# Kernel optimization log

Hardware: AMD Instinct MI355X
Metric: run time of the kernel (lower is better)

The kernel has to match this reference:

```python
import jax, jax.numpy as jnp
import numpy as np

B, N, D_IN, D_OUT, E = 2, 50000, 64, 64, 800000
EPS = 0.0


def setup_inputs() -> dict:
    key = jax.random.key(0)
    ks = jax.random.split(key, 6)
    x = jax.random.normal(ks[0], (B, N, D_IN), dtype=jnp.float32)
    edge_index = jax.random.randint(ks[1], (2, E), 0, N, dtype=jnp.int64)
    # Linear params stored as [in, out] so y = h @ W + b (same math as torch Linear)
    W1 = jax.random.normal(ks[2], (D_IN, D_OUT), dtype=jnp.float32) * (1.0 / np.sqrt(D_IN))
    b1 = jax.random.normal(ks[3], (D_OUT,), dtype=jnp.float32) * 0.01
    W2 = jax.random.normal(ks[4], (D_OUT, D_OUT), dtype=jnp.float32) * (1.0 / np.sqrt(D_OUT))
    b2 = jax.random.normal(ks[5], (D_OUT,), dtype=jnp.float32) * 0.01
    return {"x": x, "edge_index": edge_index, "W1": W1, "b1": b1, "W2": W2, "b2": b2}


def reference(x, edge_index, W1, b1, W2, b2):
    src, dst = edge_index[0], edge_index[1]
    # GIN aggregation: agg[b, d] += x[b, s] for every edge (s, d), vectorized
    # gather messages [B, E, D] then scatter-add into [B, N, D]
    agg = jnp.zeros_like(x).at[:, dst].add(x[:, src])
    h = (1.0 + EPS) * x + agg
    h = jax.nn.relu(h @ W1 + b1)
    out = h @ W2 + b2
    return out
```

## Files before the change

kernel.cpp:

```cpp
#include <hip/hip_runtime.h>


#define N_NODES 50000
#define N_EDGES 800000
#define DIM 64
#define NROWS (2 * N_NODES)
#define CAP 64
#define CSTRIDE 16

#define WS_PAD_NEEDED  22400000u
#define WS_BF16_NEEDED 19400704u
#define WS_CAP_NEEDED  13000704u

typedef __attribute__((ext_vector_type(8))) short bf16x8;
typedef __attribute__((ext_vector_type(4))) float f32x4;

__device__ __forceinline__ float rlanef(float v, int l) {
    return __int_as_float(__builtin_amdgcn_readlane(__float_as_int(v), l));
}
__device__ __forceinline__ short f2bf(float f) {
    unsigned u = __float_as_uint(f);
    return (short)((u + 0x7FFFu + ((u >> 16) & 1u)) >> 16);
}
__device__ __forceinline__ unsigned pack2bf(float lo, float hi) {
    return (unsigned)(unsigned short)f2bf(lo) | ((unsigned)(unsigned short)f2bf(hi) << 16);
}

__global__ __launch_bounds__(256)
void k_fill_cap_cvt(const int* __restrict__ ei, const float* __restrict__ x,
                    unsigned* __restrict__ counts,
                    unsigned short* __restrict__ adj,
                    unsigned* __restrict__ xbp) {
    const int tid = blockIdx.x * 256 + threadIdx.x;

    const float4 f0 = reinterpret_cast<const float4*>(x)[tid * 2];
    const float4 f1 = reinterpret_cast<const float4*>(x)[tid * 2 + 1];
    uint4 p;
    p.x = pack2bf(f0.x, f0.y);
    p.y = pack2bf(f0.z, f0.w);
    p.z = pack2bf(f1.x, f1.y);
    p.w = pack2bf(f1.z, f1.w);
    reinterpret_cast<uint4*>(xbp)[tid] = p;

    if (tid < N_EDGES) {
        int s = ei[tid];
        int d = ei[N_EDGES + tid];
        unsigned pos = atomicAdd(&counts[(size_t)d * CSTRIDE], 1u);
        if (pos < CAP) adj[(size_t)d * CAP + pos] = (unsigned short)s;
    }
}

__global__ __launch_bounds__(256, 8)
void k_gather_cap_bf16(const float* __restrict__ x,
                       const unsigned* __restrict__ xbp,
                       const unsigned* __restrict__ counts,
                       const unsigned short* __restrict__ adj,
                       float* __restrict__ out) {
    const int t = threadIdx.x;
    const int lane = t & 63;
    const int wave = t >> 6;
    const int node0 = (blockIdx.x * 4 + wave) * 4;

    const int half = lane >> 5;
    const int dpq  = lane & 31;
    const size_t bro = (size_t)half * N_NODES;

#define ULO(u) __uint_as_float((u) << 16)
#define UHI(u) __uint_as_float((u) & 0xFFFF0000u)

    #pragma unroll
    for (int j = 0; j < 4; ++j) {
        const int d = node0 + j;
        unsigned c = counts[(size_t)d * CSTRIDE];
        if (c > (unsigned)CAP) c = CAP;
        unsigned iv = 0u;
        if ((unsigned)lane < c)
            iv = (unsigned)adj[(size_t)d * CAP + lane];

        const float2 sv = *reinterpret_cast<const float2*>(
            x + (bro + (size_t)d) * DIM + dpq * 2);
        float ax = sv.x, ay = sv.y;

        for (unsigned k = 0; k < c; k += 8u) {
            const unsigned i0 = (unsigned)__builtin_amdgcn_readlane((int)iv, k);
            const unsigned i1 = (unsigned)__builtin_amdgcn_readlane((int)iv, k + 1);
            const unsigned i2 = (unsigned)__builtin_amdgcn_readlane((int)iv, k + 2);
            const unsigned i3 = (unsigned)__builtin_amdgcn_readlane((int)iv, k + 3);
            const unsigned i4 = (unsigned)__builtin_amdgcn_readlane((int)iv, k + 4);
            const unsigned i5 = (unsigned)__builtin_amdgcn_readlane((int)iv, k + 5);
            const unsigned i6 = (unsigned)__builtin_amdgcn_readlane((int)iv, k + 6);
            const unsigned i7 = (unsigned)__builtin_amdgcn_readlane((int)iv, k + 7);
            unsigned u0 = xbp[(bro + (size_t)i0) * 32 + dpq];
            unsigned u1 = xbp[(bro + (size_t)i1) * 32 + dpq];
            unsigned u2 = xbp[(bro + (size_t)i2) * 32 + dpq];
            unsigned u3 = xbp[(bro + (size_t)i3) * 32 + dpq];
            unsigned u4 = xbp[(bro + (size_t)i4) * 32 + dpq];
            unsigned u5 = xbp[(bro + (size_t)i5) * 32 + dpq];
            unsigned u6 = xbp[(bro + (size_t)i6) * 32 + dpq];
            unsigned u7 = xbp[(bro + (size_t)i7) * 32 + dpq];
            if (k + 1u >= c) u1 = 0u;
            if (k + 2u >= c) u2 = 0u;
            if (k + 3u >= c) u3 = 0u;
            if (k + 4u >= c) u4 = 0u;
            if (k + 5u >= c) u5 = 0u;
            if (k + 6u >= c) u6 = 0u;
            if (k + 7u >= c) u7 = 0u;
            ax += ((ULO(u0) + ULO(u1)) + (ULO(u2) + ULO(u3)))
                + ((ULO(u4) + ULO(u5)) + (ULO(u6) + ULO(u7)));
            ay += ((UHI(u0) + UHI(u1)) + (UHI(u2) + UHI(u3)))
                + ((UHI(u4) + UHI(u5)) + (UHI(u6) + UHI(u7)));
        }

        float2 r; r.x = ax; r.y = ay;
        *reinterpret_cast<float2*>(out + (bro + (size_t)d) * DIM + dpq * 2) = r;
    }
#undef ULO
#undef UHI
}

#define LPAD 72

__global__ __launch_bounds__(512)
void k_mlp_mfma(float* __restrict__ buf,
                const float* __restrict__ W1, const float* __restrict__ b1,
                const float* __restrict__ W2, const float* __restrict__ b2) {
    __shared__ short w1T[DIM * LPAD];
    __shared__ short w2T[DIM * LPAD];
    __shared__ float b1s[DIM], b2s[DIM];
    __shared__ short hT[8 * 16 * LPAD];

    const int t = threadIdx.x;
    for (int i = t; i < DIM * DIM; i += 512) {
        const int k = i >> 6, n = i & 63;
        w1T[n * LPAD + k] = f2bf(W1[i]);
        w2T[n * LPAD + k] = f2bf(W2[i]);
    }
    if (t < DIM) { b1s[t] = b1[t]; b2s[t] = b2[t]; }
    __syncthreads();

    const int lane = t & 63;
    const int wave = t >> 6;
    const int base = (blockIdx.x * 8 + wave) * 16;
    if (base >= NROWS) return;

    short* __restrict__ hw = hT + wave * 16 * LPAD;
    const int arow = lane & 15;
    const int kb   = (lane >> 4) * 8;
    const int crow = (lane >> 4) * 4;

    const float* hp = buf + (size_t)(base + arow) * DIM + kb;
    float4 u0 = *(const float4*)(hp);
    float4 u1 = *(const float4*)(hp + 4);
    float4 u2 = *(const float4*)(hp + 32);
    float4 u3 = *(const float4*)(hp + 36);
    bf16x8 a0, a1;
    a0[0] = f2bf(u0.x); a0[1] = f2bf(u0.y); a0[2] = f2bf(u0.z); a0[3] = f2bf(u0.w);
    a0[4] = f2bf(u1.x); a0[5] = f2bf(u1.y); a0[6] = f2bf(u1.z); a0[7] = f2bf(u1.w);
    a1[0] = f2bf(u2.x); a1[1] = f2bf(u2.y); a1[2] = f2bf(u2.z); a1[3] = f2bf(u2.w);
    a1[4] = f2bf(u3.x); a1[5] = f2bf(u3.y); a1[6] = f2bf(u3.z); a1[7] = f2bf(u3.w);

    #pragma unroll
    for (int nt = 0; nt < 4; ++nt) {
        const int col = nt * 16 + arow;
        const bf16x8 b0 = *(const bf16x8*)(w1T + col * LPAD + kb);
        const bf16x8 b1f = *(const bf16x8*)(w1T + col * LPAD + kb + 32);
        f32x4 acc = {0.f, 0.f, 0.f, 0.f};
        acc = __builtin_amdgcn_mfma_f32_16x16x32_bf16(a0, b0, acc, 0, 0, 0);
        acc = __builtin_amdgcn_mfma_f32_16x16x32_bf16(a1, b1f, acc, 0, 0, 0);
        const float bv = b1s[col];
        #pragma unroll
        for (int r = 0; r < 4; ++r) {
            float hv = fmaxf(acc[r] + bv, 0.0f);
            hw[(crow + r) * LPAD + col] = f2bf(hv);
        }
    }

    asm volatile("s_waitcnt lgkmcnt(0)" ::: "memory");
    __builtin_amdgcn_sched_barrier(0);

    const bf16x8 c0 = *(const bf16x8*)(hw + arow * LPAD + kb);
    const bf16x8 c1 = *(const bf16x8*)(hw + arow * LPAD + kb + 32);
    #pragma unroll
    for (int nt = 0; nt < 4; ++nt) {
        const int col = nt * 16 + arow;
        const bf16x8 b0 = *(const bf16x8*)(w2T + col * LPAD + kb);
        const bf16x8 b1f = *(const bf16x8*)(w2T + col * LPAD + kb + 32);
        f32x4 acc = {0.f, 0.f, 0.f, 0.f};
        acc = __builtin_amdgcn_mfma_f32_16x16x32_bf16(c0, b0, acc, 0, 0, 0);
        acc = __builtin_amdgcn_mfma_f32_16x16x32_bf16(c1, b1f, acc, 0, 0, 0);
        const float bv = b2s[col];
        #pragma unroll
        for (int r = 0; r < 4; ++r)
            buf[(size_t)(base + crow + r) * DIM + col] = acc[r] + bv;
    }
}

__global__ __launch_bounds__(256)
void k_fill_cap_cvt_r13(const int* __restrict__ ei, const float* __restrict__ x,
                        unsigned* __restrict__ counts,
                        unsigned short* __restrict__ adj,
                        unsigned* __restrict__ xbp) {
    const int tid = blockIdx.x * 256 + threadIdx.x;
    const float4 f0 = reinterpret_cast<const float4*>(x)[tid * 2];
    const float4 f1 = reinterpret_cast<const float4*>(x)[tid * 2 + 1];
    uint4 p;
    p.x = pack2bf(f0.x, f0.y);
    p.y = pack2bf(f0.z, f0.w);
    p.z = pack2bf(f1.x, f1.y);
    p.w = pack2bf(f1.z, f1.w);
    reinterpret_cast<uint4*>(xbp)[tid] = p;
    if (tid < N_EDGES) {
        int s = ei[tid];
        int d = ei[N_EDGES + tid];
        unsigned pos = atomicAdd(&counts[d], 1u);
        if (pos < CAP) adj[(size_t)d * CAP + pos] = (unsigned short)s;
    }
}

__global__ __launch_bounds__(256, 8)
void k_gather_cap_bf16_r13(const float* __restrict__ x,
                           const unsigned* __restrict__ xbp,
                           const unsigned* __restrict__ counts,
                           const unsigned short* __restrict__ adj,
                           float* __restrict__ out) {
    const int t = threadIdx.x;
    const int lane = t & 63;
    const int wave = t >> 6;
    const int node0 = (blockIdx.x * 4 + wave) * 4;
    const int half = lane >> 5;
    const int dpq  = lane & 31;
    const size_t bro = (size_t)half * N_NODES;
#define ULO(u) __uint_as_float((u) << 16)
#define UHI(u) __uint_as_float((u) & 0xFFFF0000u)
    #pragma unroll
    for (int j = 0; j < 4; ++j) {
        const int d = node0 + j;
        unsigned c = counts[d];
        if (c > (unsigned)CAP) c = CAP;
        unsigned iv = 0u;
        if ((unsigned)lane < c) iv = (unsigned)adj[(size_t)d * CAP + lane];
        const float2 sv = *reinterpret_cast<const float2*>(
            x + (bro + (size_t)d) * DIM + dpq * 2);
        float ax = sv.x, ay = sv.y;
        for (unsigned k = 0; k < c; k += 8u) {
            const unsigned i0 = (unsigned)__builtin_amdgcn_readlane((int)iv, k);
            const unsigned i1 = (unsigned)__builtin_amdgcn_readlane((int)iv, k + 1);
            const unsigned i2 = (unsigned)__builtin_amdgcn_readlane((int)iv, k + 2);
            const unsigned i3 = (unsigned)__builtin_amdgcn_readlane((int)iv, k + 3);
            const unsigned i4 = (unsigned)__builtin_amdgcn_readlane((int)iv, k + 4);
            const unsigned i5 = (unsigned)__builtin_amdgcn_readlane((int)iv, k + 5);
            const unsigned i6 = (unsigned)__builtin_amdgcn_readlane((int)iv, k + 6);
            const unsigned i7 = (unsigned)__builtin_amdgcn_readlane((int)iv, k + 7);
            unsigned u0 = xbp[(bro + (size_t)i0) * 32 + dpq];
            unsigned u1 = xbp[(bro + (size_t)i1) * 32 + dpq];
            unsigned u2 = xbp[(bro + (size_t)i2) * 32 + dpq];
            unsigned u3 = xbp[(bro + (size_t)i3) * 32 + dpq];
            unsigned u4 = xbp[(bro + (size_t)i4) * 32 + dpq];
            unsigned u5 = xbp[(bro + (size_t)i5) * 32 + dpq];
            unsigned u6 = xbp[(bro + (size_t)i6) * 32 + dpq];
            unsigned u7 = xbp[(bro + (size_t)i7) * 32 + dpq];
            if (k + 1u >= c) u1 = 0u;
            if (k + 2u >= c) u2 = 0u;
            if (k + 3u >= c) u3 = 0u;
            if (k + 4u >= c) u4 = 0u;
            if (k + 5u >= c) u5 = 0u;
            if (k + 6u >= c) u6 = 0u;
            if (k + 7u >= c) u7 = 0u;
            ax += ((ULO(u0) + ULO(u1)) + (ULO(u2) + ULO(u3)))
                + ((ULO(u4) + ULO(u5)) + (ULO(u6) + ULO(u7)));
            ay += ((UHI(u0) + UHI(u1)) + (UHI(u2) + UHI(u3)))
                + ((UHI(u4) + UHI(u5)) + (UHI(u6) + UHI(u7)));
        }
        float2 r; r.x = ax; r.y = ay;
        *reinterpret_cast<float2*>(out + (bro + (size_t)d) * DIM + dpq * 2) = r;
    }
#undef ULO
#undef UHI
}

__global__ __launch_bounds__(256)
void gin_scatter(const float* __restrict__ x, const int* __restrict__ ei,
                 float* __restrict__ agg) {
    unsigned tid = blockIdx.x * 256u + threadIdx.x;
    unsigned e = tid >> 5;
    if (e >= N_EDGES) return;
    unsigned d = (tid & 31u) * 2u;
    int s = ei[e];
    int dst = ei[N_EDGES + e];
    const float2 v0 = *reinterpret_cast<const float2*>(x + (size_t)s * DIM + d);
    float* a0 = agg + (size_t)dst * DIM + d;
    unsafeAtomicAdd(a0, v0.x);
    unsafeAtomicAdd(a0 + 1, v0.y);
    const float2 v1 = *reinterpret_cast<const float2*>(x + (size_t)(N_NODES + s) * DIM + d);
    float* a1 = agg + (size_t)(N_NODES + dst) * DIM + d;
    unsafeAtomicAdd(a1, v1.x);
    unsafeAtomicAdd(a1 + 1, v1.y);
}

__global__ __launch_bounds__(256)
void gin_mlp(float* __restrict__ buf,
             const float* __restrict__ W1, const float* __restrict__ b1,
             const float* __restrict__ W2, const float* __restrict__ b2) {
    __shared__ float w1s[DIM * DIM];
    __shared__ float w2s[DIM * DIM];
    __shared__ float b1sF[DIM], b2sF[DIM];
    const int t = threadIdx.x;
    for (int i = t; i < 1024; i += 256) {
        reinterpret_cast<float4*>(w1s)[i] = reinterpret_cast<const float4*>(W1)[i];
        reinterpret_cast<float4*>(w2s)[i] = reinterpret_cast<const float4*>(W2)[i];
    }
    if (t < DIM) { b1sF[t] = b1[t]; b2sF[t] = b2[t]; }
    __syncthreads();
    const int lane = t & 63;
    const int wave = t >> 6;
    const size_t row0 = ((size_t)blockIdx.x * 4 + wave) * 8;
    float xr[8], h[8], o[8];
    #pragma unroll
    for (int j = 0; j < 8; ++j) xr[j] = buf[(row0 + j) * DIM + lane];
    #pragma unroll
    for (int j = 0; j < 8; ++j) h[j] = b1sF[lane];
    #pragma unroll
    for (int k = 0; k < DIM; ++k) {
        float w = w1s[k * DIM + lane];
        #pragma unroll
        for (int j = 0; j < 8; ++j) h[j] = fmaf(rlanef(xr[j], k), w, h[j]);
    }
    #pragma unroll
    for (int j = 0; j < 8; ++j) h[j] = fmaxf(h[j], 0.0f);
    #pragma unroll
    for (int j = 0; j < 8; ++j) o[j] = b2sF[lane];
    #pragma unroll
    for (int k = 0; k < DIM; ++k) {
        float w = w2s[k * DIM + lane];
        #pragma unroll
        for (int j = 0; j < 8; ++j) o[j] = fmaf(rlanef(h[j], k), w, o[j]);
    }
    #pragma unroll
    for (int j = 0; j < 8; ++j) buf[(row0 + j) * DIM + lane] = o[j];
}

extern "C" void kernel_launch(void* const* d_in, const int* in_sizes, int n_in,
                              void* d_out, int out_size, void* d_ws, size_t ws_size,
                              hipStream_t stream) {
    const float* x  = (const float*)d_in[0];
    const int*   ei = (const int*)d_in[1];
    const float* W1 = (const float*)d_in[2];
    const float* b1 = (const float*)d_in[3];
    const float* W2 = (const float*)d_in[4];
    const float* b2 = (const float*)d_in[5];
    float* out = (float*)d_out;

    if (ws_size >= WS_PAD_NEEDED) {
        unsigned*       counts = (unsigned*)d_ws;
        unsigned short* adj16  = (unsigned short*)((char*)d_ws + 3200000);
        unsigned*       xbp    = (unsigned*)((char*)d_ws + 9600000);
        hipMemsetAsync(counts, 0, 3200000, stream);
        k_fill_cap_cvt<<<3125, 256, 0, stream>>>(ei, x, counts, adj16, xbp);
        k_gather_cap_bf16<<<N_NODES / 16, 256, 0, stream>>>(x, xbp, counts, adj16, out);
        k_mlp_mfma<<<(NROWS + 127) / 128, 512, 0, stream>>>(out, W1, b1, W2, b2);
    } else if (ws_size >= WS_BF16_NEEDED) {
        unsigned*       counts = (unsigned*)d_ws;
        unsigned short* adj16  = (unsigned short*)((char*)d_ws + 200704);
        unsigned*       xbp    = (unsigned*)((char*)d_ws + 6600704);
        hipMemsetAsync(counts, 0, N_NODES * sizeof(unsigned), stream);
        k_fill_cap_cvt_r13<<<3125, 256, 0, stream>>>(ei, x, counts, adj16, xbp);
        k_gather_cap_bf16_r13<<<N_NODES / 16, 256, 0, stream>>>(x, xbp, counts, adj16, out);
        k_mlp_mfma<<<(NROWS + 127) / 128, 512, 0, stream>>>(out, W1, b1, W2, b2);
    } else {
        hipMemcpyAsync(out, x, sizeof(float) * (size_t)NROWS * DIM,
                       hipMemcpyDeviceToDevice, stream);
        gin_scatter<<<(N_EDGES * 32 + 255) / 256, 256, 0, stream>>>(x, ei, out);
        gin_mlp<<<NROWS / 32, 256, 0, stream>>>(out, W1, b1, W2, b2);
    }
}
```

Before: 103.5 us.

## Fuse neighbor gather with MFMA MLP, keeping aggregated rows in LDS

The separate gather and MLP kernels are merged into one kernel. Each 512-thread block aggregates 64 nodes for both batches and writes the sums as packed bf16 into shared memory, then runs the two bf16 MFMA layers directly from LDS and writes only the final output. This removes the fp32 round trip of the aggregated tensor through global memory and one kernel launch. In exchange, every block repeats the weight transpose and conversion, LDS use per block grows, and the gather loop is no longer unrolled. The fallback branch for medium workspace sizes is also removed.

```diff
diff --git a/kernel.cpp b/kernel.cpp
--- a/kernel.cpp
+++ b/kernel.cpp
@@ -9,15 +9,10 @@
 #define CSTRIDE 16
 
 #define WS_PAD_NEEDED  22400000u
-#define WS_BF16_NEEDED 19400704u
-#define WS_CAP_NEEDED  13000704u
 
 typedef __attribute__((ext_vector_type(8))) short bf16x8;
 typedef __attribute__((ext_vector_type(4))) float f32x4;
 
-__device__ __forceinline__ float rlanef(float v, int l) {
-    return __int_as_float(__builtin_amdgcn_readlane(__float_as_int(v), l));
-}
 __device__ __forceinline__ short f2bf(float f) {
     unsigned u = __float_as_uint(f);
     return (short)((u + 0x7FFFu + ((u >> 16) & 1u)) >> 16);
@@ -50,27 +45,46 @@
     }
 }
 
-__global__ __launch_bounds__(256, 8)
-void k_gather_cap_bf16(const float* __restrict__ x,
-                       const unsigned* __restrict__ xbp,
-                       const unsigned* __restrict__ counts,
-                       const unsigned short* __restrict__ adj,
-                       float* __restrict__ out) {
+#define LPAD 72
+
+__global__ __launch_bounds__(512, 4)
+void k_gather_mlp_fused(const float* __restrict__ x,
+                        const unsigned* __restrict__ xbp,
+                        const unsigned* __restrict__ counts,
+                        const unsigned short* __restrict__ adj,
+                        const float* __restrict__ W1, const float* __restrict__ b1,
+                        const float* __restrict__ W2, const float* __restrict__ b2,
+                        float* __restrict__ out) {
+    __shared__ short w1T[DIM * LPAD];
+    __shared__ short w2T[DIM * LPAD];
+    __shared__ float b1s[DIM], b2s[DIM];
+    __shared__ unsigned hL[128 * (LPAD / 2)];
+    __shared__ short hT[8 * 16 * LPAD];
+
     const int t = threadIdx.x;
+    for (int i = t; i < DIM * DIM; i += 512) {
+        const int k = i >> 6, n = i & 63;
+        w1T[n * LPAD + k] = f2bf(W1[i]);
+        w2T[n * LPAD + k] = f2bf(W2[i]);
+    }
+    if (t < DIM) { b1s[t] = b1[t]; b2s[t] = b2[t]; }
+    __syncthreads();
+
     const int lane = t & 63;
     const int wave = t >> 6;
-    const int node0 = (blockIdx.x * 4 + wave) * 4;
 
     const int half = lane >> 5;
     const int dpq  = lane & 31;
     const size_t bro = (size_t)half * N_NODES;
+    const int nbase = blockIdx.x * 64 + wave * 8;
 
 #define ULO(u) __uint_as_float((u) << 16)
 #define UHI(u) __uint_as_float((u) & 0xFFFF0000u)
 
-    #pragma unroll
-    for (int j = 0; j < 4; ++j) {
-        const int d = node0 + j;
+    #pragma unroll 1
+    for (int j = 0; j < 8; ++j) {
+        const int d = nbase + j;
+        if (d >= N_NODES) break;
         unsigned c = counts[(size_t)d * CSTRIDE];
         if (c > (unsigned)CAP) c = CAP;
         unsigned iv = 0u;
@@ -111,53 +125,22 @@
                 + ((UHI(u4) + UHI(u5)) + (UHI(u6) + UHI(u7)));
         }
 
-        float2 r; r.x = ax; r.y = ay;
-        *reinterpret_cast<float2*>(out + (bro + (size_t)d) * DIM + dpq * 2) = r;
+        hL[(wave * 16 + j * 2 + half) * (LPAD / 2) + dpq] = pack2bf(ax, ay);
     }
 #undef ULO
 #undef UHI
-}
-
-#define LPAD 72
-
-__global__ __launch_bounds__(512)
-void k_mlp_mfma(float* __restrict__ buf,
-                const float* __restrict__ W1, const float* __restrict__ b1,
-                const float* __restrict__ W2, const float* __restrict__ b2) {
-    __shared__ short w1T[DIM * LPAD];
-    __shared__ short w2T[DIM * LPAD];
-    __shared__ float b1s[DIM], b2s[DIM];
-    __shared__ short hT[8 * 16 * LPAD];
-
-    const int t = threadIdx.x;
-    for (int i = t; i < DIM * DIM; i += 512) {
-        const int k = i >> 6, n = i & 63;
-        w1T[n * LPAD + k] = f2bf(W1[i]);
-        w2T[n * LPAD + k] = f2bf(W2[i]);
-    }
-    if (t < DIM) { b1s[t] = b1[t]; b2s[t] = b2[t]; }
-    __syncthreads();
-
-    const int lane = t & 63;
-    const int wave = t >> 6;
-    const int base = (blockIdx.x * 8 + wave) * 16;
-    if (base >= NROWS) return;
+
+    asm volatile("s_waitcnt lgkmcnt(0)" ::: "memory");
+    __builtin_amdgcn_sched_barrier(0);
 
     short* __restrict__ hw = hT + wave * 16 * LPAD;
+    const unsigned* __restrict__ hrow = hL + (size_t)wave * 16 * (LPAD / 2);
     const int arow = lane & 15;
     const int kb   = (lane >> 4) * 8;
     const int crow = (lane >> 4) * 4;
 
-    const float* hp = buf + (size_t)(base + arow) * DIM + kb;
-    float4 u0 = *(const float4*)(hp);
-    float4 u1 = *(const float4*)(hp + 4);
-    float4 u2 = *(const float4*)(hp + 32);
-    float4 u3 = *(const float4*)(hp + 36);
-    bf16x8 a0, a1;
-    a0[0] = f2bf(u0.x); a0[1] = f2bf(u0.y); a0[2] = f2bf(u0.z); a0[3] = f2bf(u0.w);
-    a0[4] = f2bf(u1.x); a0[5] = f2bf(u1.y); a0[6] = f2bf(u1.z); a0[7] = f2bf(u1.w);
-    a1[0] = f2bf(u2.x); a1[1] = f2bf(u2.y); a1[2] = f2bf(u2.z); a1[3] = f2bf(u2.w);
-    a1[4] = f2bf(u3.x); a1[5] = f2bf(u3.y); a1[6] = f2bf(u3.z); a1[7] = f2bf(u3.w);
+    const bf16x8 a0 = *(const bf16x8*)(hrow + arow * (LPAD / 2) + (kb >> 1));
+    const bf16x8 a1 = *(const bf16x8*)(hrow + arow * (LPAD / 2) + (kb >> 1) + 16);
 
     #pragma unroll
     for (int nt = 0; nt < 4; ++nt) {
@@ -190,92 +173,18 @@
         acc = __builtin_amdgcn_mfma_f32_16x16x32_bf16(c1, b1f, acc, 0, 0, 0);
         const float bv = b2s[col];
         #pragma unroll
-        for (int r = 0; r < 4; ++r)
-            buf[(size_t)(base + crow + r) * DIM + col] = acc[r] + bv;
-    }
-}
-
-__global__ __launch_bounds__(256)
-void k_fill_cap_cvt_r13(const int* __restrict__ ei, const float* __restrict__ x,
-                        unsigned* __restrict__ counts,
-                        unsigned short* __restrict__ adj,
-                        unsigned* __restrict__ xbp) {
-    const int tid = blockIdx.x * 256 + threadIdx.x;
-    const float4 f0 = reinterpret_cast<const float4*>(x)[tid * 2];
-    const float4 f1 = reinterpret_cast<const float4*>(x)[tid * 2 + 1];
-    uint4 p;
-    p.x = pack2bf(f0.x, f0.y);
-    p.y = pack2bf(f0.z, f0.w);
-    p.z = pack2bf(f1.x, f1.y);
-    p.w = pack2bf(f1.z, f1.w);
-    reinterpret_cast<uint4*>(xbp)[tid] = p;
-    if (tid < N_EDGES) {
-        int s = ei[tid];
-        int d = ei[N_EDGES + tid];
-        unsigned pos = atomicAdd(&counts[d], 1u);
-        if (pos < CAP) adj[(size_t)d * CAP + pos] = (unsigned short)s;
-    }
-}
-
-__global__ __launch_bounds__(256, 8)
-void k_gather_cap_bf16_r13(const float* __restrict__ x,
-                           const unsigned* __restrict__ xbp,
-                           const unsigned* __restrict__ counts,
-                           const unsigned short* __restrict__ adj,
-                           float* __restrict__ out) {
-    const int t = threadIdx.x;
-    const int lane = t & 63;
-    const int wave = t >> 6;
-    const int node0 = (blockIdx.x * 4 + wave) * 4;
-    const int half = lane >> 5;
-    const int dpq  = lane & 31;
-    const size_t bro = (size_t)half * N_NODES;
-#define ULO(u) __uint_as_float((u) << 16)
-#define UHI(u) __uint_as_float((u) & 0xFFFF0000u)
-    #pragma unroll
-    for (int j = 0; j < 4; ++j) {
-        const int d = node0 + j;
-        unsigned c = counts[d];
-        if (c > (unsigned)CAP) c = CAP;
-        unsigned iv = 0u;
-        if ((unsigned)lane < c) iv = (unsigned)adj[(size_t)d * CAP + lane];
-        const float2 sv = *reinterpret_cast<const float2*>(
-            x + (bro + (size_t)d) * DIM + dpq * 2);
-        float ax = sv.x, ay = sv.y;
-        for (unsigned k = 0; k < c; k += 8u) {
-            const unsigned i0 = (unsigned)__builtin_amdgcn_readlane((int)iv, k);
-            const unsigned i1 = (unsigned)__builtin_amdgcn_readlane((int)iv, k + 1);
-            const unsigned i2 = (unsigned)__builtin_amdgcn_readlane((int)iv, k + 2);
-            const unsigned i3 = (unsigned)__builtin_amdgcn_readlane((int)iv, k + 3);
-            const unsigned i4 = (unsigned)__builtin_amdgcn_readlane((int)iv, k + 4);
-            const unsigned i5 = (unsigned)__builtin_amdgcn_readlane((int)iv, k + 5);
-            const unsigned i6 = (unsigned)__builtin_amdgcn_readlane((int)iv, k + 6);
-            const unsigned i7 = (unsigned)__builtin_amdgcn_readlane((int)iv, k + 7);
-            unsigned u0 = xbp[(bro + (size_t)i0) * 32 + dpq];
-            unsigned u1 = xbp[(bro + (size_t)i1) * 32 + dpq];
-            unsigned u2 = xbp[(bro + (size_t)i2) * 32 + dpq];
-            unsigned u3 = xbp[(bro + (size_t)i3) * 32 + dpq];
-            unsigned u4 = xbp[(bro + (size_t)i4) * 32 + dpq];
-            unsigned u5 = xbp[(bro + (size_t)i5) * 32 + dpq];
-            unsigned u6 = xbp[(bro + (size_t)i6) * 32 + dpq];
-            unsigned u7 = xbp[(bro + (size_t)i7) * 32 + dpq];
-            if (k + 1u >= c) u1 = 0u;
-            if (k + 2u >= c) u2 = 0u;
-            if (k + 3u >= c) u3 = 0u;
-            if (k + 4u >= c) u4 = 0u;
-            if (k + 5u >= c) u5 = 0u;
-            if (k + 6u >= c) u6 = 0u;
-            if (k + 7u >= c) u7 = 0u;
-            ax += ((ULO(u0) + ULO(u1)) + (ULO(u2) + ULO(u3)))
-                + ((ULO(u4) + ULO(u5)) + (ULO(u6) + ULO(u7)));
-            ay += ((UHI(u0) + UHI(u1)) + (UHI(u2) + UHI(u3)))
-                + ((UHI(u4) + UHI(u5)) + (UHI(u6) + UHI(u7)));
+        for (int r = 0; r < 4; ++r) {
+            const int rblk = wave * 16 + crow + r;
+            const int node = blockIdx.x * 64 + (rblk >> 1);
+            if (node < N_NODES)
+                out[((size_t)(rblk & 1) * N_NODES + (size_t)node) * DIM + col]
+                    = acc[r] + bv;
         }
-        float2 r; r.x = ax; r.y = ay;
-        *reinterpret_cast<float2*>(out + (bro + (size_t)d) * DIM + dpq * 2) = r;
-    }
-#undef ULO
-#undef UHI
+    }
+}
+
+__device__ __forceinline__ float rlanef(float v, int l) {
+    return __int_as_float(__builtin_amdgcn_readlane(__float_as_int(v), l));
 }
 
 __global__ __launch_bounds__(256)
@@ -356,16 +265,8 @@
         unsigned*       xbp    = (unsigned*)((char*)d_ws + 9600000);
         hipMemsetAsync(counts, 0, 3200000, stream);
         k_fill_cap_cvt<<<3125, 256, 0, stream>>>(ei, x, counts, adj16, xbp);
-        k_gather_cap_bf16<<<N_NODES / 16, 256, 0, stream>>>(x, xbp, counts, adj16, out);
-        k_mlp_mfma<<<(NROWS + 127) / 128, 512, 0, stream>>>(out, W1, b1, W2, b2);
-    } else if (ws_size >= WS_BF16_NEEDED) {
-        unsigned*       counts = (unsigned*)d_ws;
-        unsigned short* adj16  = (unsigned short*)((char*)d_ws + 200704);
-        unsigned*       xbp    = (unsigned*)((char*)d_ws + 6600704);
-        hipMemsetAsync(counts, 0, N_NODES * sizeof(unsigned), stream);
-        k_fill_cap_cvt_r13<<<3125, 256, 0, stream>>>(ei, x, counts, adj16, xbp);
-        k_gather_cap_bf16_r13<<<N_NODES / 16, 256, 0, stream>>>(x, xbp, counts, adj16, out);
-        k_mlp_mfma<<<(NROWS + 127) / 128, 512, 0, stream>>>(out, W1, b1, W2, b2);
+        k_gather_mlp_fused<<<(N_NODES + 63) / 64, 512, 0, stream>>>(
+            x, xbp, counts, adj16, W1, b1, W2, b2, out);
     } else {
         hipMemcpyAsync(out, x, sizeof(float) * (size_t)NROWS * DIM,
                        hipMemcpyDeviceToDevice, stream);
```

Result: slower. 115.4 us (+11.5%).
